# Kernel optimization log

Hardware: AMD Instinct MI355X
Metric: run time of the kernel (lower is better)

The kernel has to match this reference:

```python
import jax, jax.numpy as jnp
import numpy as np

N = 100000  # nodes
E = 1600000  # edges (without self-loops)


def _gcn_norm(edge_index, n):
    # add self loops, compute symmetric normalization D^-1/2 (A+I) D^-1/2
    loops = jnp.arange(n, dtype=edge_index.dtype)
    src = jnp.concatenate([edge_index[0], loops])
    dst = jnp.concatenate([edge_index[1], loops])
    deg = jax.ops.segment_sum(jnp.ones_like(dst, dtype=jnp.float32), dst, num_segments=n)
    dinv = jax.lax.rsqrt(jnp.maximum(deg, 1.0))  # deg >= 1 due to self loops
    norm = dinv[src] * dinv[dst]  # [E+N]
    return src, dst, norm


def _gcn_layer(x, W, b, src, dst, norm, n):
    h = x @ W  # [N, out]
    msg = h[src] * norm[:, None]  # [E+N, out]
    agg = jax.ops.segment_sum(msg, dst, num_segments=n)
    return agg + b


def setup_inputs() -> dict:
    key = jax.random.key(0)
    ks = jax.random.split(key, 8)
    x = jax.random.normal(ks[0], (N, 256), dtype=jnp.float32)
    edge_index = jax.random.randint(ks[1], (2, E), 0, N, dtype=jnp.int32)
    W1 = jax.random.normal(ks[2], (256, 128), dtype=jnp.float32) / np.sqrt(256.0)
    b1 = jnp.zeros((128,), dtype=jnp.float32)
    W2 = jax.random.normal(ks[3], (128, 128), dtype=jnp.float32) / np.sqrt(128.0)
    b2 = jnp.zeros((128,), dtype=jnp.float32)
    W3 = jax.random.normal(ks[4], (128, 16), dtype=jnp.float32) / np.sqrt(128.0)
    b3 = jnp.zeros((16,), dtype=jnp.float32)
    return {"x": x, "edge_index": edge_index, "W1": W1, "b1": b1,
            "W2": W2, "b2": b2, "W3": W3, "b3": b3}


def reference(x, edge_index, W1, b1, W2, b2, W3, b3):
    n = x.shape[0]
    src, dst, norm = _gcn_norm(edge_index, n)
    h = jax.nn.relu(_gcn_layer(x, W1, b1, src, dst, norm, n))
    # dropout layers are identity in eval mode
    h = jax.nn.relu(_gcn_layer(h, W2, b2, src, dst, norm, n))
    out = _gcn_layer(h, W3, b3, src, dst, norm, n)
    return out
```

## Files before the change

### kernel.cpp

```cpp
#include <hip/hip_runtime.h>
#include <hip/hip_bf16.h>
#include <cstdint>
#include <cstddef>

typedef __hip_bfloat16 bf16;

typedef __attribute__((ext_vector_type(8))) short s16x8;
typedef __attribute__((ext_vector_type(4))) float f32x4;
typedef __attribute__((ext_vector_type(8))) unsigned short u16x8;

__device__ __forceinline__ float bflo(unsigned u) { return __uint_as_float(u << 16); }
__device__ __forceinline__ float bfhi(unsigned u) { return __uint_as_float(u & 0xffff0000u); }
__device__ __forceinline__ unsigned packbf2(float a, float b) {
  unsigned lo = (unsigned)__bfloat16_as_ushort(__float2bfloat16(a));
  unsigned hi = (unsigned)__bfloat16_as_ushort(__float2bfloat16(b));
  return lo | (hi << 16);
}
__device__ __forceinline__ float to_f(float v) { return v; }
__device__ __forceinline__ float to_f(bf16 v) { return __bfloat162float(v); }

__device__ __forceinline__ void gload_lds16(const void* g, void* l) {
  __builtin_amdgcn_global_load_lds((const __attribute__((address_space(1))) unsigned int*)g,
                                   (__attribute__((address_space(3))) unsigned int*)l, 16, 0, 0);
}

__global__ __launch_bounds__(256) void k_detect(const unsigned* __restrict__ x, int* __restrict__ flag,
                                                int forced) {
  __shared__ int sm[256];
  int t = threadIdx.x;
  if (forced >= 0) { if (t == 0) *flag = forced; return; }
  int cnt = 0;
  for (int i = t; i < 4096; i += 256) {
    unsigned u = x[i];
    unsigned lo_exp = (u >> 7) & 0xFF;
    cnt += (lo_exp >= 97 && lo_exp <= 130) ? 1 : 0;
  }
  sm[t] = cnt;
  __syncthreads();
  for (int off = 128; off > 0; off >>= 1) {
    if (t < off) sm[t] += sm[t + off];
    __syncthreads();
  }
  if (t == 0) *flag = (sm[0] > 2048) ? 1 : 0;
}


__global__ __launch_bounds__(256) void k_init(int* fil, int* rcur, int n) {
  int i = blockIdx.x * 256 + threadIdx.x;
  if (i < n) fil[i] = 0;
  if (blockIdx.x == 0 && threadIdx.x < 8) rcur[threadIdx.x] = 0;
}

template <int P>
__global__ __launch_bounds__(256) void k_bin(const int* __restrict__ src, const int* __restrict__ dst,
                                             uint2* __restrict__ stage, int* __restrict__ rcur,
                                             int* __restrict__ fil, int* __restrict__ csr,
                                             int E, int N, int rsz, int capR, int cap) {
  __shared__ int hcnt[P], hbase[P], hcur[P];
  const int t = threadIdx.x;
  const int base = blockIdx.x * 2048;
  if (t < P) hcnt[t] = 0;
  __syncthreads();
  int dloc[8], sloc[8], rloc[8];
#pragma unroll
  for (int j = 0; j < 8; ++j) {
    int e = base + j * 256 + t;
    bool valid = (e < E);
    int d = valid ? dst[e] : 0;
    int s = valid ? src[e] : 0;
    if ((unsigned)d >= (unsigned)N) valid = false;
    if ((unsigned)s >= (unsigned)N) s = 0;
    int r = valid ? (d / rsz) : -1;
    dloc[j] = d; sloc[j] = s; rloc[j] = r;
    if (valid) atomicAdd(&hcnt[r], 1);
  }
  __syncthreads();
  if (t < P) {
    hbase[t] = atomicAdd(&rcur[t], hcnt[t]);
    hcur[t] = 0;
  }
  __syncthreads();
#pragma unroll
  for (int j = 0; j < 8; ++j) {
    int r = rloc[j];
    if (r >= 0) {
      int pos = hbase[r] + atomicAdd(&hcur[r], 1);
      if (pos < capR) {
        stage[(size_t)r * capR + pos] = make_uint2((unsigned)dloc[j], (unsigned)sloc[j]);
      } else {
        int pp = atomicAdd(&fil[dloc[j]], 1);
        if (pp < cap) csr[(size_t)dloc[j] * cap + pp] = sloc[j];
      }
    }
  }
}

template <int P>
__global__ __launch_bounds__(256) void k_fillb(const uint2* __restrict__ stage, const int* __restrict__ rcur,
                                               int* __restrict__ fil, int* __restrict__ csr,
                                               int capR, int cap) {
  const int r = blockIdx.x & (P - 1);
  const int nb = gridDim.x / P;
  const int chunk = blockIdx.x / P;
  int cnt = rcur[r];
  if (cnt > capR) cnt = capR;
  const uint2* sg = stage + (size_t)r * capR;
  for (int i = chunk * 256 + threadIdx.x; i < cnt; i += nb * 256) {
    uint2 e = sg[i];
    int p = atomicAdd(&fil[e.x], 1);
    if (p < cap) csr[(size_t)e.x * cap + p] = (int)e.y;
  }
}

__global__ __launch_bounds__(256) void k_dinv(const int* __restrict__ fil, float* __restrict__ dinv, int n) {
  int i = blockIdx.x * 256 + threadIdx.x;
  if (i < n) dinv[i] = rsqrtf((float)fil[i] + 1.0f);
}

template <typename TB, int WANT, int SPLIT>
__global__ __launch_bounds__(256) void k_packB(const int* __restrict__ flag,
                                               const TB* __restrict__ B,
                                               unsigned short* __restrict__ Bp, int K) {
  if (*flag != WANT) return;
  const int nf = (K >> 5) * 512;
  int t = blockIdx.x * 256 + threadIdx.x;
  if (t >= nf) return;
  int s = t >> 9, rem = t & 511, c = rem >> 6, l = rem & 63;
  int kb = (s << 5) + ((l >> 4) << 3);
  int col = (c << 4) + (l & 15);
  u16x8 vh, vl;
#pragma unroll
  for (int i = 0; i < 8; ++i) {
    float f = to_f(B[(size_t)(kb + i) * 128 + col]);
    bf16 h = __float2bfloat16(f);
    vh[i] = __bfloat16_as_ushort(h);
    if (SPLIT) {
      float r = f - __bfloat162float(h);
      vl[i] = __bfloat16_as_ushort(__float2bfloat16(r));
    }
  }
  *(u16x8*)(Bp + (size_t)t * 8) = vh;
  if (SPLIT) *(u16x8*)(Bp + ((size_t)nf + t) * 8) = vl;
}

template <typename TA, int WANT, int MODE, int KT>
__global__ __launch_bounds__(256) void k_gemm_mfma(const int* __restrict__ flag,
                                                   const TA* __restrict__ A,
                                                   const unsigned short* __restrict__ Bp,
                                                   const float* __restrict__ dinv,
                                                   bf16* __restrict__ C, int M) {
  if (*flag != WANT) return;
  constexpr int steps = KT >> 5;
  constexpr int NFRAG = (MODE >= 1) ? 16 : 8;
  constexpr int FPW = NFRAG / 4;
  constexpr size_t nfbytes = (size_t)steps * 8192;
  __shared__ s16x8 lds[2][NFRAG * 64];
  const int tid = threadIdx.x;
  const int l = tid & 63;
  const int w = tid >> 6;
  const int row0 = blockIdx.x * 128 + w * 32;
  int arow0 = row0 + (l & 15);
  int arow1 = row0 + 16 + (l & 15);
  if (arow0 >= M) arow0 = M - 1;
  if (arow1 >= M) arow1 = M - 1;
  const TA* Ap0 = A + (size_t)arow0 * KT + ((l >> 4) << 3);
  const TA* Ap1 = A + (size_t)arow1 * KT + ((l >> 4) << 3);
  const char* Bb = (const char*)Bp;

  auto stage = [&](int b, int s) {
#pragma unroll
    for (int j = 0; j < FPW; ++j) {
      int q = w * FPW + j;
      size_t off = (q < 8) ? ((size_t)(s * 8 + q)) * 1024
                           : nfbytes + ((size_t)(s * 8 + q - 8)) * 1024;
      gload_lds16(Bb + off + (size_t)l * 16, (void*)&lds[b][q * 64]);
    }
  };

  f32x4 acc[2][8];
#pragma unroll
  for (int rs = 0; rs < 2; ++rs)
#pragma unroll
    for (int c = 0; c < 8; ++c) acc[rs][c] = (f32x4){0.f, 0.f, 0.f, 0.f};

  float4 f0[3], f1[3], f2[3], f3[3];
  s16x8 ra0[3], ra1[3];
  auto loadA = [&](int s, int slot) {
    if constexpr (MODE == 2) {
      const float* p0 = (const float*)(Ap0 + (s << 5));
      const float* p1 = (const float*)(Ap1 + (s << 5));
      f0[slot] = *(const float4*)p0; f1[slot] = *(const float4*)(p0 + 4);
      f2[slot] = *(const float4*)p1; f3[slot] = *(const float4*)(p1 + 4);
    } else {
      ra0[slot] = *(const s16x8*)(Ap0 + (s << 5));
      ra1[slot] = *(const s16x8*)(Ap1 + (s << 5));
    }
  };

  auto mkfrag = [&](const float4& lo4, const float4& hi4, s16x8& a, s16x8& alo) {
    float f[8] = {lo4.x, lo4.y, lo4.z, lo4.w, hi4.x, hi4.y, hi4.z, hi4.w};
#pragma unroll
    for (int i = 0; i < 8; ++i) {
      bf16 h = __float2bfloat16(f[i]);
      a[i] = (short)__bfloat16_as_ushort(h);
      float r = f[i] - __bfloat162float(h);
      alo[i] = (short)__bfloat16_as_ushort(__float2bfloat16(r));
    }
  };

  stage(0, 0);
  __builtin_amdgcn_sched_barrier(0);
  loadA(0, 0);
  if constexpr (steps > 1) loadA(1, 1);
  if constexpr (MODE == 2) asm volatile("s_waitcnt vmcnt(8)" ::: "memory");
  else                     asm volatile("s_waitcnt vmcnt(4)" ::: "memory");
  __builtin_amdgcn_s_barrier();
  __builtin_amdgcn_sched_barrier(0);

#pragma unroll
  for (int s = 0; s < steps; ++s) {
    const int b = s & 1;
    if (s + 1 < steps) stage(b ^ 1, s + 1);
    __builtin_amdgcn_sched_barrier(0);
    if (s + 2 < steps) loadA(s + 2, (s + 2) % 3);
    s16x8 a0, alo0, a1, alo1;
    if constexpr (MODE == 2) {
      const int sl = s % 3;
      mkfrag(f0[sl], f1[sl], a0, alo0);
      mkfrag(f2[sl], f3[sl], a1, alo1);
    } else {
      a0 = ra0[s % 3];
      a1 = ra1[s % 3];
    }
#pragma unroll
    for (int c = 0; c < 8; ++c) {
      s16x8 bh = lds[b][c * 64 + l];
      acc[0][c] = __builtin_amdgcn_mfma_f32_16x16x32_bf16(a0, bh, acc[0][c], 0, 0, 0);
      acc[1][c] = __builtin_amdgcn_mfma_f32_16x16x32_bf16(a1, bh, acc[1][c], 0, 0, 0);
      if constexpr (MODE >= 1) {
        s16x8 bl = lds[b][(8 + c) * 64 + l];
        acc[0][c] = __builtin_amdgcn_mfma_f32_16x16x32_bf16(a0, bl, acc[0][c], 0, 0, 0);
        acc[1][c] = __builtin_amdgcn_mfma_f32_16x16x32_bf16(a1, bl, acc[1][c], 0, 0, 0);
      }
      if constexpr (MODE == 2) {
        acc[0][c] = __builtin_amdgcn_mfma_f32_16x16x32_bf16(alo0, bh, acc[0][c], 0, 0, 0);
        acc[1][c] = __builtin_amdgcn_mfma_f32_16x16x32_bf16(alo1, bh, acc[1][c], 0, 0, 0);
      }
    }
    if (s + 1 < steps) {
      if (s + 2 < steps) {
        if constexpr (MODE == 2) asm volatile("s_waitcnt vmcnt(4)" ::: "memory");
        else                     asm volatile("s_waitcnt vmcnt(2)" ::: "memory");
      } else {
        asm volatile("s_waitcnt vmcnt(0)" ::: "memory");
      }
      __builtin_amdgcn_s_barrier();
      __builtin_amdgcn_sched_barrier(0);
    }
  }

  const int lb = l & 15;
#pragma unroll
  for (int rs = 0; rs < 2; ++rs) {
    const int rbase = row0 + rs * 16 + ((l >> 4) << 2);
#pragma unroll
    for (int r = 0; r < 4; ++r) {
      int row = rbase + r;
      if (row < M) {
        float sc = dinv[row];
        bf16* Cr = C + (size_t)row * 128 + lb;
#pragma unroll
        for (int c = 0; c < 8; ++c) Cr[c << 4] = __float2bfloat16(acc[rs][c][r] * sc);
      }
    }
  }
}

template <typename TB, int WANT>
__global__ __launch_bounds__(256) void k_gemm16(const int* __restrict__ flag,
                                                const bf16* __restrict__ A, const TB* __restrict__ B,
                                                const float* __restrict__ dinv, float* __restrict__ C, int M) {
  if (*flag != WANT) return;
  __shared__ float Bs[128][16];
  const int tid = threadIdx.x;
  for (int l = tid; l < 128 * 16; l += 256) Bs[l >> 4][l & 15] = to_f(B[l]);
  __syncthreads();
  const int r = blockIdx.x * 64 + (tid >> 2);
  const int c0 = (tid & 3) * 4;
  if (r >= M) return;
  const bf16* Ar = A + (size_t)r * 128;
  float a0 = 0.f, a1 = 0.f, a2 = 0.f, a3 = 0.f;
#pragma unroll
  for (int k = 0; k < 128; k += 8) {
    uint4 u = *(const uint4*)&Ar[k];
    float f[8] = {bflo(u.x), bfhi(u.x), bflo(u.y), bfhi(u.y),
                  bflo(u.z), bfhi(u.z), bflo(u.w), bfhi(u.w)};
#pragma unroll
    for (int j = 0; j < 8; ++j) {
      float4 b = *(const float4*)&Bs[k + j][c0];
      a0 = fmaf(f[j], b.x, a0); a1 = fmaf(f[j], b.y, a1);
      a2 = fmaf(f[j], b.z, a2); a3 = fmaf(f[j], b.w, a3);
    }
  }
  float s = dinv[r];
  *(float4*)&C[(size_t)r * 16 + c0] = make_float4(a0 * s, a1 * s, a2 * s, a3 * s);
}


template <typename TB, int WANT>
__global__ __launch_bounds__(256) void k_agg128(const int* __restrict__ flag,
                                                const bf16* __restrict__ Hs, const int* __restrict__ deg,
                                                const int* __restrict__ csr, const float* __restrict__ dinv,
                                                const TB* __restrict__ bias, bf16* __restrict__ out,
                                                int M, int cap) {
  if (*flag != WANT) return;
  const int wid = threadIdx.x >> 6, lane = threadIdx.x & 63;
  const int node = blockIdx.x * 4 + wid;
  if (node >= M) return;
  const int g = lane >> 4, li = lane & 15;
  int dg = deg[node];
  if (dg > cap) dg = cap;
  const int* ce = csr + (size_t)node * cap;
  const int total = dg + 1;
  float acc[8];
#pragma unroll
  for (int i = 0; i < 8; ++i) acc[i] = 0.f;

  auto rowsrc = [&](int k) -> int {
    return (k == 0) ? node : ce[k - 1];
  };
  auto addu4 = [&](uint4 u) {
    acc[0] += bflo(u.x); acc[1] += bfhi(u.x);
    acc[2] += bflo(u.y); acc[3] += bfhi(u.y);
    acc[4] += bflo(u.z); acc[5] += bfhi(u.z);
    acc[6] += bflo(u.w); acc[7] += bfhi(u.w);
  };

  int base = 0;
  for (; base + 8 <= total; base += 8) {
    int s0 = rowsrc(base + g);
    int s1 = rowsrc(base + 4 + g);
    uint4 u0 = *(const uint4*)(Hs + (size_t)s0 * 128 + li * 8);
    uint4 u1 = *(const uint4*)(Hs + (size_t)s1 * 128 + li * 8);
    addu4(u0); addu4(u1);
  }
  for (; base < total; base += 4) {
    int k = base + g;
    bool v = (k < total);
    int s = v ? rowsrc(k) : node;
    uint4 u = *(const uint4*)(Hs + (size_t)s * 128 + li * 8);
    if (v) addu4(u);
  }

#pragma unroll
  for (int i = 0; i < 8; ++i) {
    acc[i] += __shfl_xor(acc[i], 16);
    acc[i] += __shfl_xor(acc[i], 32);
  }

  if (lane < 16) {
    float di = dinv[node];
    const int c0 = li * 8;
    float o[8];
#pragma unroll
    for (int i = 0; i < 8; ++i) o[i] = fmaxf(acc[i] * di + to_f(bias[c0 + i]), 0.f);
    uint4 ov;
    ov.x = packbf2(o[0], o[1]);
    ov.y = packbf2(o[2], o[3]);
    ov.z = packbf2(o[4], o[5]);
    ov.w = packbf2(o[6], o[7]);
    *(uint4*)(out + (size_t)node * 128 + c0) = ov;
  }
}

template <typename TB, typename TO, int WANT>
__global__ __launch_bounds__(256) void k_agg16(const int* __restrict__ flag,
                                               const float* __restrict__ Hs, const int* __restrict__ deg,
                                               const int* __restrict__ csr, const float* __restrict__ dinv,
                                               const TB* __restrict__ bias, TO* __restrict__ out,
                                               int M, int cap) {
  if (*flag != WANT) return;
  int sub = threadIdx.x >> 4, lane = threadIdx.x & 15;
  int node = blockIdx.x * 16 + sub;
  if (node >= M) return;
  float acc = Hs[(size_t)node * 16 + lane];
  int dg = deg[node];
  if (dg > cap) dg = cap;
  const int* ce = csr + (size_t)node * cap;
  int e = 0;
  for (; e + 8 <= dg; e += 8) {
    int s0 = ce[e],     s1 = ce[e + 1], s2 = ce[e + 2], s3 = ce[e + 3];
    int s4 = ce[e + 4], s5 = ce[e + 5], s6 = ce[e + 6], s7 = ce[e + 7];
    acc += (Hs[(size_t)s0 * 16 + lane] + Hs[(size_t)s1 * 16 + lane]) +
           (Hs[(size_t)s2 * 16 + lane] + Hs[(size_t)s3 * 16 + lane]) +
           (Hs[(size_t)s4 * 16 + lane] + Hs[(size_t)s5 * 16 + lane]) +
           (Hs[(size_t)s6 * 16 + lane] + Hs[(size_t)s7 * 16 + lane]);
  }
  for (; e + 4 <= dg; e += 4) {
    int s0 = ce[e], s1 = ce[e + 1], s2 = ce[e + 2], s3 = ce[e + 3];
    acc += Hs[(size_t)s0 * 16 + lane] + Hs[(size_t)s1 * 16 + lane] +
           Hs[(size_t)s2 * 16 + lane] + Hs[(size_t)s3 * 16 + lane];
  }
  for (; e < dg; ++e) acc += Hs[(size_t)ce[e] * 16 + lane];
  float o = acc * dinv[node] + to_f(bias[lane]);
  out[(size_t)node * 16 + lane] = (TO)o;
}


extern "C" void kernel_launch(void* const* d_in, const int* in_sizes, int n_in,
                              void* d_out, int out_size, void* d_ws, size_t ws_size,
                              hipStream_t stream) {
  const int* ei = (const int*)d_in[1];

  const long long w1sz = in_sizes[2];
  const int kmode = (int)(w1sz / 32768);
  const int N = (int)((long long)in_sizes[0] * 128 / w1sz);
  const int E = (kmode == 1) ? in_sizes[1] / 2 : in_sizes[1] / 8;
  const int forced = (kmode == 2) ? 1 : (kmode == 4) ? 0 : -1;
  const int* srcv = ei;
  const int* dstv = ei + E;

  long long meandeg = (N > 0) ? (long long)E / N : 0;
  int cap = (int)((4 * meandeg + 15) & ~15LL);
  if (cap < 64) cap = 64;

  char* p = (char*)d_ws;
  auto alloc = [&](size_t b) { char* r = p; p += (b + 255) & ~(size_t)255; return r; };
  int*   flag   = (int*)alloc(256);
  int*   rcur   = (int*)alloc(256);
  int*   fil    = (int*)alloc((size_t)N * 4);
  float* dinv   = (float*)alloc((size_t)N * 4);
  int*   csr    = (int*)alloc((size_t)N * cap * 4);
  bf16*  HsB    = (bf16*)alloc((size_t)N * 128 * 2);
  bf16*  hB     = (bf16*)alloc((size_t)N * 128 * 2);
  unsigned short* Bp1 = (unsigned short*)alloc(131072);
  unsigned short* Bp2 = (unsigned short*)alloc(65536);
  float* Hs16   = (float*)HsB;
  uint2* stg    = (uint2*)HsB;
  const int capR = N * 4;

  const int gN = (N + 255) / 256;
  k_detect<<<1, 256, 0, stream>>>((const unsigned*)d_in[0], flag, forced);
  k_init <<<gN, 256, 0, stream>>>(fil, rcur, N);
  {
    constexpr int P = 8;
    const int rsz = (N + P - 1) / P;
    const int nch = (E + 2047) / 2048;
    k_bin<P>  <<<nch, 256, 0, stream>>>(srcv, dstv, stg, rcur, fil, csr, E, N, rsz, capR, cap);
    k_fillb<P><<<1024, 256, 0, stream>>>(stg, rcur, fil, csr, capR, cap);
  }
  k_dinv <<<gN, 256, 0, stream>>>(fil, dinv, N);

  const int gM128 = (N + 127) / 128;
  const int gM64  = (N + 63) / 64;
  const int gAgg  = (N + 3) / 4;
  const bool doB16 = (forced != 0);
  const bool doF32 = (forced != 1);

  if (doB16) {
    const bf16* x  = (const bf16*)d_in[0];
    const bf16* b1 = (const bf16*)d_in[3];
    const bf16* b2 = (const bf16*)d_in[5];
    const bf16* W3 = (const bf16*)d_in[6]; const bf16* b3 = (const bf16*)d_in[7];
    k_packB<bf16, 1, 0><<<16, 256, 0, stream>>>(flag, (const bf16*)d_in[2], Bp1, 256);
    k_packB<bf16, 1, 0><<<8,  256, 0, stream>>>(flag, (const bf16*)d_in[4], Bp2, 128);
    k_gemm_mfma<bf16, 1, 0, 256><<<gM128, 256, 0, stream>>>(flag, x, Bp1, dinv, HsB, N);
    k_agg128<bf16, 1><<<gAgg, 256, 0, stream>>>(flag, HsB, fil, csr, dinv, b1, hB, N, cap);
    k_gemm_mfma<bf16, 1, 0, 128><<<gM128, 256, 0, stream>>>(flag, hB, Bp2, dinv, HsB, N);
    k_agg128<bf16, 1><<<gAgg, 256, 0, stream>>>(flag, HsB, fil, csr, dinv, b2, hB, N, cap);
    k_gemm16<bf16, 1><<<gM64, 256, 0, stream>>>(flag, hB, W3, dinv, Hs16, N);
    k_agg16<bf16, bf16, 1><<<(N + 15) / 16, 256, 0, stream>>>(flag, Hs16, fil, csr, dinv, b3,
                                                              (bf16*)d_out, N, cap);
  }
  if (doF32) {
    const float* x  = (const float*)d_in[0];
    const float* b1 = (const float*)d_in[3];
    const float* b2 = (const float*)d_in[5];
    const float* W3 = (const float*)d_in[6]; const float* b3 = (const float*)d_in[7];
    k_packB<float, 0, 1><<<16, 256, 0, stream>>>(flag, (const float*)d_in[2], Bp1, 256);
    k_packB<float, 0, 1><<<8,  256, 0, stream>>>(flag, (const float*)d_in[4], Bp2, 128);
    k_gemm_mfma<float, 0, 2, 256><<<gM128, 256, 0, stream>>>(flag, x, Bp1, dinv, HsB, N);
    k_agg128<float, 0><<<gAgg, 256, 0, stream>>>(flag, HsB, fil, csr, dinv, b1, hB, N, cap);
    k_gemm_mfma<bf16, 0, 1, 128><<<gM128, 256, 0, stream>>>(flag, hB, Bp2, dinv, HsB, N);
    k_agg128<float, 0><<<gAgg, 256, 0, stream>>>(flag, HsB, fil, csr, dinv, b2, hB, N, cap);
    k_gemm16<float, 0><<<gM64, 256, 0, stream>>>(flag, hB, W3, dinv, Hs16, N);
    k_agg16<float, float, 0><<<(N + 15) / 16, 256, 0, stream>>>(flag, Hs16, fil, csr, dinv, b3,
                                                                (float*)d_out, N, cap);
  }
}
```

Baseline: 493.3 us.

## Fuse layer-1 GEMM with edge binning and move dinv scaling into aggregation

Layer 1's GEMM no longer depends on dinv: the per-row source scaling moves from the GEMM epilogue into the aggregation kernels, which now multiply each gathered row by dinv[src]. That lets the first GEMM run in the same grid as the edge-binning kernel, so compute-bound and atomic-bound work overlap. The duplicated bf16 and f32 launch sequences become a single sequence that branches on the device flag inside each kernel, and the two weight-packing kernels are merged into one, cutting the launch count roughly in half. In exchange, aggregation does an extra dinv gather per edge, and the binning stage buffer moves to hB so the GEMM output can live in HsB.

```diff
diff --git a/kernel.cpp b/kernel.cpp
--- a/kernel.cpp
+++ b/kernel.cpp
@@ -44,21 +44,176 @@
   if (t == 0) *flag = (sm[0] > 2048) ? 1 : 0;
 }
 
-
 __global__ __launch_bounds__(256) void k_init(int* fil, int* rcur, int n) {
   int i = blockIdx.x * 256 + threadIdx.x;
   if (i < n) fil[i] = 0;
   if (blockIdx.x == 0 && threadIdx.x < 8) rcur[threadIdx.x] = 0;
 }
 
+__device__ __forceinline__ void pack_body(const void* Bsrc, unsigned short* Bp, int K,
+                                          int isb, int t) {
+  const int nf = (K >> 5) * 512;
+  if (t >= nf) return;
+  int s = t >> 9, rem = t & 511, c = rem >> 6, l = rem & 63;
+  int kb = (s << 5) + ((l >> 4) << 3);
+  int col = (c << 4) + (l & 15);
+  u16x8 vh, vl;
+#pragma unroll
+  for (int i = 0; i < 8; ++i) {
+    float f = isb ? to_f(((const bf16*)Bsrc)[(size_t)(kb + i) * 128 + col])
+                  : ((const float*)Bsrc)[(size_t)(kb + i) * 128 + col];
+    bf16 h = __float2bfloat16(f);
+    vh[i] = __bfloat16_as_ushort(h);
+    float r = f - __bfloat162float(h);
+    vl[i] = __bfloat16_as_ushort(__float2bfloat16(r));
+  }
+  *(u16x8*)(Bp + (size_t)t * 8) = vh;
+  if (!isb) *(u16x8*)(Bp + ((size_t)nf + t) * 8) = vl;
+}
+
+__global__ __launch_bounds__(256) void k_pack(const int* __restrict__ flag,
+                                              const void* __restrict__ B1, const void* __restrict__ B2,
+                                              unsigned short* __restrict__ Bp1,
+                                              unsigned short* __restrict__ Bp2) {
+  const int isb = (*flag == 1);
+  if (blockIdx.x < 16) pack_body(B1, Bp1, 256, isb, blockIdx.x * 256 + threadIdx.x);
+  else                 pack_body(B2, Bp2, 128, isb, (blockIdx.x - 16) * 256 + threadIdx.x);
+}
+
+template <typename TA, int MODE, int KT>
+__device__ void gemm_body(const TA* __restrict__ A, const unsigned short* __restrict__ Bp,
+                          bf16* __restrict__ C, int M, int blk, s16x8* ldsbuf) {
+  constexpr int steps = KT >> 5;
+  constexpr int NFRAG = (MODE >= 1) ? 16 : 8;
+  constexpr int FPW = NFRAG / 4;
+  constexpr size_t nfbytes = (size_t)steps * 8192;
+  const int tid = threadIdx.x;
+  const int l = tid & 63;
+  const int w = tid >> 6;
+  const int row0 = blk * 128 + w * 32;
+  int arow0 = row0 + (l & 15);
+  int arow1 = row0 + 16 + (l & 15);
+  if (arow0 >= M) arow0 = M - 1;
+  if (arow1 >= M) arow1 = M - 1;
+  const TA* Ap0 = A + (size_t)arow0 * KT + ((l >> 4) << 3);
+  const TA* Ap1 = A + (size_t)arow1 * KT + ((l >> 4) << 3);
+  const char* Bb = (const char*)Bp;
+
+  auto stage = [&](int b, int s) {
+#pragma unroll
+    for (int j = 0; j < FPW; ++j) {
+      int q = w * FPW + j;
+      size_t off = (q < 8) ? ((size_t)(s * 8 + q)) * 1024
+                           : nfbytes + ((size_t)(s * 8 + q - 8)) * 1024;
+      gload_lds16(Bb + off + (size_t)l * 16, (void*)&ldsbuf[b * (NFRAG * 64) + q * 64]);
+    }
+  };
+
+  f32x4 acc[2][8];
+#pragma unroll
+  for (int rs = 0; rs < 2; ++rs)
+#pragma unroll
+    for (int c = 0; c < 8; ++c) acc[rs][c] = (f32x4){0.f, 0.f, 0.f, 0.f};
+
+  float4 f0[3], f1[3], f2[3], f3[3];
+  s16x8 ra0[3], ra1[3];
+  auto loadA = [&](int s, int slot) {
+    if constexpr (MODE == 2) {
+      const float* p0 = (const float*)(Ap0 + (s << 5));
+      const float* p1 = (const float*)(Ap1 + (s << 5));
+      f0[slot] = *(const float4*)p0; f1[slot] = *(const float4*)(p0 + 4);
+      f2[slot] = *(const float4*)p1; f3[slot] = *(const float4*)(p1 + 4);
+    } else {
+      ra0[slot] = *(const s16x8*)(Ap0 + (s << 5));
+      ra1[slot] = *(const s16x8*)(Ap1 + (s << 5));
+    }
+  };
+  auto mkfrag = [&](const float4& lo4, const float4& hi4, s16x8& a, s16x8& alo) {
+    float f[8] = {lo4.x, lo4.y, lo4.z, lo4.w, hi4.x, hi4.y, hi4.z, hi4.w};
+#pragma unroll
+    for (int i = 0; i < 8; ++i) {
+      bf16 h = __float2bfloat16(f[i]);
+      a[i] = (short)__bfloat16_as_ushort(h);
+      float r = f[i] - __bfloat162float(h);
+      alo[i] = (short)__bfloat16_as_ushort(__float2bfloat16(r));
+    }
+  };
+
+  stage(0, 0);
+  __builtin_amdgcn_sched_barrier(0);
+  loadA(0, 0);
+  if constexpr (steps > 1) loadA(1, 1);
+  if constexpr (MODE == 2) asm volatile("s_waitcnt vmcnt(8)" ::: "memory");
+  else                     asm volatile("s_waitcnt vmcnt(4)" ::: "memory");
+  __builtin_amdgcn_s_barrier();
+  __builtin_amdgcn_sched_barrier(0);
+
+#pragma unroll
+  for (int s = 0; s < steps; ++s) {
+    const int b = s & 1;
+    if (s + 1 < steps) stage(b ^ 1, s + 1);
+    __builtin_amdgcn_sched_barrier(0);
+    if (s + 2 < steps) loadA(s + 2, (s + 2) % 3);
+    s16x8 a0, alo0, a1, alo1;
+    if constexpr (MODE == 2) {
+      const int sl = s % 3;
+      mkfrag(f0[sl], f1[sl], a0, alo0);
+      mkfrag(f2[sl], f3[sl], a1, alo1);
+    } else {
+      a0 = ra0[s % 3];
+      a1 = ra1[s % 3];
+    }
+#pragma unroll
+    for (int c = 0; c < 8; ++c) {
+      s16x8 bh = ldsbuf[b * (NFRAG * 64) + c * 64 + l];
+      acc[0][c] = __builtin_amdgcn_mfma_f32_16x16x32_bf16(a0, bh, acc[0][c], 0, 0, 0);
+      acc[1][c] = __builtin_amdgcn_mfma_f32_16x16x32_bf16(a1, bh, acc[1][c], 0, 0, 0);
+      if constexpr (MODE >= 1) {
+        s16x8 bl = ldsbuf[b * (NFRAG * 64) + (8 + c) * 64 + l];
+        acc[0][c] = __builtin_amdgcn_mfma_f32_16x16x32_bf16(a0, bl, acc[0][c], 0, 0, 0);
+        acc[1][c] = __builtin_amdgcn_mfma_f32_16x16x32_bf16(a1, bl, acc[1][c], 0, 0, 0);
+      }
+      if constexpr (MODE == 2) {
+        acc[0][c] = __builtin_amdgcn_mfma_f32_16x16x32_bf16(alo0, bh, acc[0][c], 0, 0, 0);
+        acc[1][c] = __builtin_amdgcn_mfma_f32_16x16x32_bf16(alo1, bh, acc[1][c], 0, 0, 0);
+      }
+    }
+    if (s + 1 < steps) {
+      if (s + 2 < steps) {
+        if constexpr (MODE == 2) asm volatile("s_waitcnt vmcnt(4)" ::: "memory");
+        else                     asm volatile("s_waitcnt vmcnt(2)" ::: "memory");
+      } else {
+        asm volatile("s_waitcnt vmcnt(0)" ::: "memory");
+      }
+      __builtin_amdgcn_s_barrier();
+      __builtin_amdgcn_sched_barrier(0);
+    }
+  }
+
+  const int lb = l & 15;
+#pragma unroll
+  for (int rs = 0; rs < 2; ++rs) {
+    const int rbase = row0 + rs * 16 + ((l >> 4) << 2);
+#pragma unroll
+    for (int r = 0; r < 4; ++r) {
+      int row = rbase + r;
+      if (row < M) {
+        bf16* Cr = C + (size_t)row * 128 + lb;
+#pragma unroll
+        for (int c = 0; c < 8; ++c) Cr[c << 4] = __float2bfloat16(acc[rs][c][r]);
+      }
+    }
+  }
+}
+
 template <int P>
-__global__ __launch_bounds__(256) void k_bin(const int* __restrict__ src, const int* __restrict__ dst,
-                                             uint2* __restrict__ stage, int* __restrict__ rcur,
-                                             int* __restrict__ fil, int* __restrict__ csr,
-                                             int E, int N, int rsz, int capR, int cap) {
-  __shared__ int hcnt[P], hbase[P], hcur[P];
+__device__ void bin_body(const int* __restrict__ src, const int* __restrict__ dst,
+                         uint2* __restrict__ stage, int* __restrict__ rcur,
+                         int* __restrict__ fil, int* __restrict__ csr,
+                         int E, int N, int rsz, int capR, int cap, int bid,
+                         int* hcnt, int* hbase, int* hcur) {
   const int t = threadIdx.x;
-  const int base = blockIdx.x * 2048;
+  const int base = bid * 2048;
   if (t < P) hcnt[t] = 0;
   __syncthreads();
   int dloc[8], sloc[8], rloc[8];
@@ -93,6 +248,36 @@
       }
     }
   }
+}
+
+template <int P>
+__global__ __launch_bounds__(256) void k_g1bin(const int* __restrict__ flag,
+                                               const void* __restrict__ A,
+                                               const unsigned short* __restrict__ Bp1,
+                                               bf16* __restrict__ C, int M,
+                                               const int* __restrict__ src, const int* __restrict__ dst,
+                                               uint2* __restrict__ stage, int* __restrict__ rcur,
+                                               int* __restrict__ fil, int* __restrict__ csr,
+                                               int E, int N, int rsz, int capR, int cap,
+                                               int gemmBlocks) {
+  __shared__ s16x8 lds[2 * 16 * 64];
+  __shared__ int hcnt[P], hbase[P], hcur[P];
+  if ((int)blockIdx.x < gemmBlocks) {
+    if (*flag == 1) gemm_body<bf16, 0, 256>((const bf16*)A, Bp1, C, M, blockIdx.x, lds);
+    else            gemm_body<float, 2, 256>((const float*)A, Bp1, C, M, blockIdx.x, lds);
+  } else {
+    bin_body<P>(src, dst, stage, rcur, fil, csr, E, N, rsz, capR, cap,
+                blockIdx.x - gemmBlocks, hcnt, hbase, hcur);
+  }
+}
+
+__global__ __launch_bounds__(256) void k_gemm2(const int* __restrict__ flag,
+                                               const bf16* __restrict__ A,
+                                               const unsigned short* __restrict__ Bp2,
+                                               bf16* __restrict__ C, int M) {
+  __shared__ s16x8 lds[2 * 16 * 64];
+  if (*flag == 1) gemm_body<bf16, 0, 128>(A, Bp2, C, M, blockIdx.x, lds);
+  else            gemm_body<bf16, 1, 128>(A, Bp2, C, M, blockIdx.x, lds);
 }
 
 template <int P>
@@ -117,203 +302,12 @@
   if (i < n) dinv[i] = rsqrtf((float)fil[i] + 1.0f);
 }
 
-template <typename TB, int WANT, int SPLIT>
-__global__ __launch_bounds__(256) void k_packB(const int* __restrict__ flag,
-                                               const TB* __restrict__ B,
-                                               unsigned short* __restrict__ Bp, int K) {
-  if (*flag != WANT) return;
-  const int nf = (K >> 5) * 512;
-  int t = blockIdx.x * 256 + threadIdx.x;
-  if (t >= nf) return;
-  int s = t >> 9, rem = t & 511, c = rem >> 6, l = rem & 63;
-  int kb = (s << 5) + ((l >> 4) << 3);
-  int col = (c << 4) + (l & 15);
-  u16x8 vh, vl;
-#pragma unroll
-  for (int i = 0; i < 8; ++i) {
-    float f = to_f(B[(size_t)(kb + i) * 128 + col]);
-    bf16 h = __float2bfloat16(f);
-    vh[i] = __bfloat16_as_ushort(h);
-    if (SPLIT) {
-      float r = f - __bfloat162float(h);
-      vl[i] = __bfloat16_as_ushort(__float2bfloat16(r));
-    }
-  }
-  *(u16x8*)(Bp + (size_t)t * 8) = vh;
-  if (SPLIT) *(u16x8*)(Bp + ((size_t)nf + t) * 8) = vl;
-}
-
-template <typename TA, int WANT, int MODE, int KT>
-__global__ __launch_bounds__(256) void k_gemm_mfma(const int* __restrict__ flag,
-                                                   const TA* __restrict__ A,
-                                                   const unsigned short* __restrict__ Bp,
-                                                   const float* __restrict__ dinv,
-                                                   bf16* __restrict__ C, int M) {
-  if (*flag != WANT) return;
-  constexpr int steps = KT >> 5;
-  constexpr int NFRAG = (MODE >= 1) ? 16 : 8;
-  constexpr int FPW = NFRAG / 4;
-  constexpr size_t nfbytes = (size_t)steps * 8192;
-  __shared__ s16x8 lds[2][NFRAG * 64];
-  const int tid = threadIdx.x;
-  const int l = tid & 63;
-  const int w = tid >> 6;
-  const int row0 = blockIdx.x * 128 + w * 32;
-  int arow0 = row0 + (l & 15);
-  int arow1 = row0 + 16 + (l & 15);
-  if (arow0 >= M) arow0 = M - 1;
-  if (arow1 >= M) arow1 = M - 1;
-  const TA* Ap0 = A + (size_t)arow0 * KT + ((l >> 4) << 3);
-  const TA* Ap1 = A + (size_t)arow1 * KT + ((l >> 4) << 3);
-  const char* Bb = (const char*)Bp;
-
-  auto stage = [&](int b, int s) {
-#pragma unroll
-    for (int j = 0; j < FPW; ++j) {
-      int q = w * FPW + j;
-      size_t off = (q < 8) ? ((size_t)(s * 8 + q)) * 1024
-                           : nfbytes + ((size_t)(s * 8 + q - 8)) * 1024;
-      gload_lds16(Bb + off + (size_t)l * 16, (void*)&lds[b][q * 64]);
-    }
-  };
-
-  f32x4 acc[2][8];
-#pragma unroll
-  for (int rs = 0; rs < 2; ++rs)
-#pragma unroll
-    for (int c = 0; c < 8; ++c) acc[rs][c] = (f32x4){0.f, 0.f, 0.f, 0.f};
-
-  float4 f0[3], f1[3], f2[3], f3[3];
-  s16x8 ra0[3], ra1[3];
-  auto loadA = [&](int s, int slot) {
-    if constexpr (MODE == 2) {
-      const float* p0 = (const float*)(Ap0 + (s << 5));
-      const float* p1 = (const float*)(Ap1 + (s << 5));
-      f0[slot] = *(const float4*)p0; f1[slot] = *(const float4*)(p0 + 4);
-      f2[slot] = *(const float4*)p1; f3[slot] = *(const float4*)(p1 + 4);
-    } else {
-      ra0[slot] = *(const s16x8*)(Ap0 + (s << 5));
-      ra1[slot] = *(const s16x8*)(Ap1 + (s << 5));
-    }
-  };
-
-  auto mkfrag = [&](const float4& lo4, const float4& hi4, s16x8& a, s16x8& alo) {
-    float f[8] = {lo4.x, lo4.y, lo4.z, lo4.w, hi4.x, hi4.y, hi4.z, hi4.w};
-#pragma unroll
-    for (int i = 0; i < 8; ++i) {
-      bf16 h = __float2bfloat16(f[i]);
-      a[i] = (short)__bfloat16_as_ushort(h);
-      float r = f[i] - __bfloat162float(h);
-      alo[i] = (short)__bfloat16_as_ushort(__float2bfloat16(r));
-    }
-  };
-
-  stage(0, 0);
-  __builtin_amdgcn_sched_barrier(0);
-  loadA(0, 0);
-  if constexpr (steps > 1) loadA(1, 1);
-  if constexpr (MODE == 2) asm volatile("s_waitcnt vmcnt(8)" ::: "memory");
-  else                     asm volatile("s_waitcnt vmcnt(4)" ::: "memory");
-  __builtin_amdgcn_s_barrier();
-  __builtin_amdgcn_sched_barrier(0);
-
-#pragma unroll
-  for (int s = 0; s < steps; ++s) {
-    const int b = s & 1;
-    if (s + 1 < steps) stage(b ^ 1, s + 1);
-    __builtin_amdgcn_sched_barrier(0);
-    if (s + 2 < steps) loadA(s + 2, (s + 2) % 3);
-    s16x8 a0, alo0, a1, alo1;
-    if constexpr (MODE == 2) {
-      const int sl = s % 3;
-      mkfrag(f0[sl], f1[sl], a0, alo0);
-      mkfrag(f2[sl], f3[sl], a1, alo1);
-    } else {
-      a0 = ra0[s % 3];
-      a1 = ra1[s % 3];
-    }
-#pragma unroll
-    for (int c = 0; c < 8; ++c) {
-      s16x8 bh = lds[b][c * 64 + l];
-      acc[0][c] = __builtin_amdgcn_mfma_f32_16x16x32_bf16(a0, bh, acc[0][c], 0, 0, 0);
-      acc[1][c] = __builtin_amdgcn_mfma_f32_16x16x32_bf16(a1, bh, acc[1][c], 0, 0, 0);
-      if constexpr (MODE >= 1) {
-        s16x8 bl = lds[b][(8 + c) * 64 + l];
-        acc[0][c] = __builtin_amdgcn_mfma_f32_16x16x32_bf16(a0, bl, acc[0][c], 0, 0, 0);
-        acc[1][c] = __builtin_amdgcn_mfma_f32_16x16x32_bf16(a1, bl, acc[1][c], 0, 0, 0);
-      }
-      if constexpr (MODE == 2) {
-        acc[0][c] = __builtin_amdgcn_mfma_f32_16x16x32_bf16(alo0, bh, acc[0][c], 0, 0, 0);
-        acc[1][c] = __builtin_amdgcn_mfma_f32_16x16x32_bf16(alo1, bh, acc[1][c], 0, 0, 0);
-      }
-    }
-    if (s + 1 < steps) {
-      if (s + 2 < steps) {
-        if constexpr (MODE == 2) asm volatile("s_waitcnt vmcnt(4)" ::: "memory");
-        else                     asm volatile("s_waitcnt vmcnt(2)" ::: "memory");
-      } else {
-        asm volatile("s_waitcnt vmcnt(0)" ::: "memory");
-      }
-      __builtin_amdgcn_s_barrier();
-      __builtin_amdgcn_sched_barrier(0);
-    }
-  }
-
-  const int lb = l & 15;
-#pragma unroll
-  for (int rs = 0; rs < 2; ++rs) {
-    const int rbase = row0 + rs * 16 + ((l >> 4) << 2);
-#pragma unroll
-    for (int r = 0; r < 4; ++r) {
-      int row = rbase + r;
-      if (row < M) {
-        float sc = dinv[row];
-        bf16* Cr = C + (size_t)row * 128 + lb;
-#pragma unroll
-        for (int c = 0; c < 8; ++c) Cr[c << 4] = __float2bfloat16(acc[rs][c][r] * sc);
-      }
-    }
-  }
-}
-
-template <typename TB, int WANT>
-__global__ __launch_bounds__(256) void k_gemm16(const int* __restrict__ flag,
-                                                const bf16* __restrict__ A, const TB* __restrict__ B,
-                                                const float* __restrict__ dinv, float* __restrict__ C, int M) {
-  if (*flag != WANT) return;
-  __shared__ float Bs[128][16];
-  const int tid = threadIdx.x;
-  for (int l = tid; l < 128 * 16; l += 256) Bs[l >> 4][l & 15] = to_f(B[l]);
-  __syncthreads();
-  const int r = blockIdx.x * 64 + (tid >> 2);
-  const int c0 = (tid & 3) * 4;
-  if (r >= M) return;
-  const bf16* Ar = A + (size_t)r * 128;
-  float a0 = 0.f, a1 = 0.f, a2 = 0.f, a3 = 0.f;
-#pragma unroll
-  for (int k = 0; k < 128; k += 8) {
-    uint4 u = *(const uint4*)&Ar[k];
-    float f[8] = {bflo(u.x), bfhi(u.x), bflo(u.y), bfhi(u.y),
-                  bflo(u.z), bfhi(u.z), bflo(u.w), bfhi(u.w)};
-#pragma unroll
-    for (int j = 0; j < 8; ++j) {
-      float4 b = *(const float4*)&Bs[k + j][c0];
-      a0 = fmaf(f[j], b.x, a0); a1 = fmaf(f[j], b.y, a1);
-      a2 = fmaf(f[j], b.z, a2); a3 = fmaf(f[j], b.w, a3);
-    }
-  }
-  float s = dinv[r];
-  *(float4*)&C[(size_t)r * 16 + c0] = make_float4(a0 * s, a1 * s, a2 * s, a3 * s);
-}
-
-
-template <typename TB, int WANT>
 __global__ __launch_bounds__(256) void k_agg128(const int* __restrict__ flag,
                                                 const bf16* __restrict__ Hs, const int* __restrict__ deg,
                                                 const int* __restrict__ csr, const float* __restrict__ dinv,
-                                                const TB* __restrict__ bias, bf16* __restrict__ out,
+                                                const void* __restrict__ bias, bf16* __restrict__ out,
                                                 int M, int cap) {
-  if (*flag != WANT) return;
+  const int isb = (*flag == 1);
   const int wid = threadIdx.x >> 6, lane = threadIdx.x & 63;
   const int node = blockIdx.x * 4 + wid;
   if (node >= M) return;
@@ -326,14 +320,12 @@
 #pragma unroll
   for (int i = 0; i < 8; ++i) acc[i] = 0.f;
 
-  auto rowsrc = [&](int k) -> int {
-    return (k == 0) ? node : ce[k - 1];
-  };
-  auto addu4 = [&](uint4 u) {
-    acc[0] += bflo(u.x); acc[1] += bfhi(u.x);
-    acc[2] += bflo(u.y); acc[3] += bfhi(u.y);
-    acc[4] += bflo(u.z); acc[5] += bfhi(u.z);
-    acc[6] += bflo(u.w); acc[7] += bfhi(u.w);
+  auto rowsrc = [&](int k) -> int { return (k == 0) ? node : ce[k - 1]; };
+  auto addu4 = [&](uint4 u, float ds) {
+    acc[0] = fmaf(bflo(u.x), ds, acc[0]); acc[1] = fmaf(bfhi(u.x), ds, acc[1]);
+    acc[2] = fmaf(bflo(u.y), ds, acc[2]); acc[3] = fmaf(bfhi(u.y), ds, acc[3]);
+    acc[4] = fmaf(bflo(u.z), ds, acc[4]); acc[5] = fmaf(bfhi(u.z), ds, acc[5]);
+    acc[6] = fmaf(bflo(u.w), ds, acc[6]); acc[7] = fmaf(bfhi(u.w), ds, acc[7]);
   };
 
   int base = 0;
@@ -342,14 +334,16 @@
     int s1 = rowsrc(base + 4 + g);
     uint4 u0 = *(const uint4*)(Hs + (size_t)s0 * 128 + li * 8);
     uint4 u1 = *(const uint4*)(Hs + (size_t)s1 * 128 + li * 8);
-    addu4(u0); addu4(u1);
+    float d0 = dinv[s0], d1 = dinv[s1];
+    addu4(u0, d0); addu4(u1, d1);
   }
   for (; base < total; base += 4) {
     int k = base + g;
     bool v = (k < total);
     int s = v ? rowsrc(k) : node;
     uint4 u = *(const uint4*)(Hs + (size_t)s * 128 + li * 8);
-    if (v) addu4(u);
+    float ds = dinv[s];
+    if (v) addu4(u, ds);
   }
 
 #pragma unroll
@@ -363,7 +357,10 @@
     const int c0 = li * 8;
     float o[8];
 #pragma unroll
-    for (int i = 0; i < 8; ++i) o[i] = fmaxf(acc[i] * di + to_f(bias[c0 + i]), 0.f);
+    for (int i = 0; i < 8; ++i) {
+      float bv = isb ? to_f(((const bf16*)bias)[c0 + i]) : ((const float*)bias)[c0 + i];
+      o[i] = fmaxf(acc[i] * di + bv, 0.f);
+    }
     uint4 ov;
     ov.x = packbf2(o[0], o[1]);
     ov.y = packbf2(o[2], o[3]);
@@ -373,37 +370,64 @@
   }
 }
 
-template <typename TB, typename TO, int WANT>
+__global__ __launch_bounds__(256) void k_gemm16(const int* __restrict__ flag,
+                                                const bf16* __restrict__ A, const void* __restrict__ B,
+                                                float* __restrict__ C, int M) {
+  const int isb = (*flag == 1);
+  __shared__ float Bs[128][16];
+  const int tid = threadIdx.x;
+  for (int l = tid; l < 128 * 16; l += 256)
+    Bs[l >> 4][l & 15] = isb ? to_f(((const bf16*)B)[l]) : ((const float*)B)[l];
+  __syncthreads();
+  const int r = blockIdx.x * 64 + (tid >> 2);
+  const int c0 = (tid & 3) * 4;
+  if (r >= M) return;
+  const bf16* Ar = A + (size_t)r * 128;
+  float a0 = 0.f, a1 = 0.f, a2 = 0.f, a3 = 0.f;
+#pragma unroll
+  for (int k = 0; k < 128; k += 8) {
+    uint4 u = *(const uint4*)&Ar[k];
+    float f[8] = {bflo(u.x), bfhi(u.x), bflo(u.y), bfhi(u.y),
+                  bflo(u.z), bfhi(u.z), bflo(u.w), bfhi(u.w)};
+#pragma unroll
+    for (int j = 0; j < 8; ++j) {
+      float4 b = *(const float4*)&Bs[k + j][c0];
+      a0 = fmaf(f[j], b.x, a0); a1 = fmaf(f[j], b.y, a1);
+      a2 = fmaf(f[j], b.z, a2); a3 = fmaf(f[j], b.w, a3);
+    }
+  }
+  *(float4*)&C[(size_t)r * 16 + c0] = make_float4(a0, a1, a2, a3);
+}
+
 __global__ __launch_bounds__(256) void k_agg16(const int* __restrict__ flag,
                                                const float* __restrict__ Hs, const int* __restrict__ deg,
                                                const int* __restrict__ csr, const float* __restrict__ dinv,
-                                               const TB* __restrict__ bias, TO* __restrict__ out,
+                                               const void* __restrict__ bias, void* __restrict__ out,
                                                int M, int cap) {
-  if (*flag != WANT) return;
+  const int isb = (*flag == 1);
   int sub = threadIdx.x >> 4, lane = threadIdx.x & 15;
   int node = blockIdx.x * 16 + sub;
   if (node >= M) return;
-  float acc = Hs[(size_t)node * 16 + lane];
+  float acc = Hs[(size_t)node * 16 + lane] * dinv[node];
   int dg = deg[node];
   if (dg > cap) dg = cap;
   const int* ce = csr + (size_t)node * cap;
   int e = 0;
-  for (; e + 8 <= dg; e += 8) {
-    int s0 = ce[e],     s1 = ce[e + 1], s2 = ce[e + 2], s3 = ce[e + 3];
-    int s4 = ce[e + 4], s5 = ce[e + 5], s6 = ce[e + 6], s7 = ce[e + 7];
-    acc += (Hs[(size_t)s0 * 16 + lane] + Hs[(size_t)s1 * 16 + lane]) +
-           (Hs[(size_t)s2 * 16 + lane] + Hs[(size_t)s3 * 16 + lane]) +
-           (Hs[(size_t)s4 * 16 + lane] + Hs[(size_t)s5 * 16 + lane]) +
-           (Hs[(size_t)s6 * 16 + lane] + Hs[(size_t)s7 * 16 + lane]);
-  }
   for (; e + 4 <= dg; e += 4) {
     int s0 = ce[e], s1 = ce[e + 1], s2 = ce[e + 2], s3 = ce[e + 3];
-    acc += Hs[(size_t)s0 * 16 + lane] + Hs[(size_t)s1 * 16 + lane] +
-           Hs[(size_t)s2 * 16 + lane] + Hs[(size_t)s3 * 16 + lane];
-  }
-  for (; e < dg; ++e) acc += Hs[(size_t)ce[e] * 16 + lane];
-  float o = acc * dinv[node] + to_f(bias[lane]);
-  out[(size_t)node * 16 + lane] = (TO)o;
+    acc = fmaf(Hs[(size_t)s0 * 16 + lane], dinv[s0], acc);
+    acc = fmaf(Hs[(size_t)s1 * 16 + lane], dinv[s1], acc);
+    acc = fmaf(Hs[(size_t)s2 * 16 + lane], dinv[s2], acc);
+    acc = fmaf(Hs[(size_t)s3 * 16 + lane], dinv[s3], acc);
+  }
+  for (; e < dg; ++e) {
+    int s = ce[e];
+    acc = fmaf(Hs[(size_t)s * 16 + lane], dinv[s], acc);
+  }
+  float bv = isb ? to_f(((const bf16*)bias)[lane]) : ((const float*)bias)[lane];
+  float o = acc * dinv[node] + bv;
+  if (isb) ((bf16*)out)[(size_t)node * 16 + lane] = (bf16)o;
+  else     ((float*)out)[(size_t)node * 16 + lane] = o;
 }
 
 
@@ -436,55 +460,28 @@
   unsigned short* Bp1 = (unsigned short*)alloc(131072);
   unsigned short* Bp2 = (unsigned short*)alloc(65536);
   float* Hs16   = (float*)HsB;
-  uint2* stg    = (uint2*)HsB;
+  uint2* stg    = (uint2*)hB;
   const int capR = N * 4;
 
   const int gN = (N + 255) / 256;
-  k_detect<<<1, 256, 0, stream>>>((const unsigned*)d_in[0], flag, forced);
-  k_init <<<gN, 256, 0, stream>>>(fil, rcur, N);
-  {
-    constexpr int P = 8;
-    const int rsz = (N + P - 1) / P;
-    const int nch = (E + 2047) / 2048;
-    k_bin<P>  <<<nch, 256, 0, stream>>>(srcv, dstv, stg, rcur, fil, csr, E, N, rsz, capR, cap);
-    k_fillb<P><<<1024, 256, 0, stream>>>(stg, rcur, fil, csr, capR, cap);
-  }
-  k_dinv <<<gN, 256, 0, stream>>>(fil, dinv, N);
-
   const int gM128 = (N + 127) / 128;
   const int gM64  = (N + 63) / 64;
   const int gAgg  = (N + 3) / 4;
-  const bool doB16 = (forced != 0);
-  const bool doF32 = (forced != 1);
-
-  if (doB16) {
-    const bf16* x  = (const bf16*)d_in[0];
-    const bf16* b1 = (const bf16*)d_in[3];
-    const bf16* b2 = (const bf16*)d_in[5];
-    const bf16* W3 = (const bf16*)d_in[6]; const bf16* b3 = (const bf16*)d_in[7];
-    k_packB<bf16, 1, 0><<<16, 256, 0, stream>>>(flag, (const bf16*)d_in[2], Bp1, 256);
-    k_packB<bf16, 1, 0><<<8,  256, 0, stream>>>(flag, (const bf16*)d_in[4], Bp2, 128);
-    k_gemm_mfma<bf16, 1, 0, 256><<<gM128, 256, 0, stream>>>(flag, x, Bp1, dinv, HsB, N);
-    k_agg128<bf16, 1><<<gAgg, 256, 0, stream>>>(flag, HsB, fil, csr, dinv, b1, hB, N, cap);
-    k_gemm_mfma<bf16, 1, 0, 128><<<gM128, 256, 0, stream>>>(flag, hB, Bp2, dinv, HsB, N);
-    k_agg128<bf16, 1><<<gAgg, 256, 0, stream>>>(flag, HsB, fil, csr, dinv, b2, hB, N, cap);
-    k_gemm16<bf16, 1><<<gM64, 256, 0, stream>>>(flag, hB, W3, dinv, Hs16, N);
-    k_agg16<bf16, bf16, 1><<<(N + 15) / 16, 256, 0, stream>>>(flag, Hs16, fil, csr, dinv, b3,
-                                                              (bf16*)d_out, N, cap);
-  }
-  if (doF32) {
-    const float* x  = (const float*)d_in[0];
-    const float* b1 = (const float*)d_in[3];
-    const float* b2 = (const float*)d_in[5];
-    const float* W3 = (const float*)d_in[6]; const float* b3 = (const float*)d_in[7];
-    k_packB<float, 0, 1><<<16, 256, 0, stream>>>(flag, (const float*)d_in[2], Bp1, 256);
-    k_packB<float, 0, 1><<<8,  256, 0, stream>>>(flag, (const float*)d_in[4], Bp2, 128);
-    k_gemm_mfma<float, 0, 2, 256><<<gM128, 256, 0, stream>>>(flag, x, Bp1, dinv, HsB, N);
-    k_agg128<float, 0><<<gAgg, 256, 0, stream>>>(flag, HsB, fil, csr, dinv, b1, hB, N, cap);
-    k_gemm_mfma<bf16, 0, 1, 128><<<gM128, 256, 0, stream>>>(flag, hB, Bp2, dinv, HsB, N);
-    k_agg128<float, 0><<<gAgg, 256, 0, stream>>>(flag, HsB, fil, csr, dinv, b2, hB, N, cap);
-    k_gemm16<float, 0><<<gM64, 256, 0, stream>>>(flag, hB, W3, dinv, Hs16, N);
-    k_agg16<float, float, 0><<<(N + 15) / 16, 256, 0, stream>>>(flag, Hs16, fil, csr, dinv, b3,
-                                                                (float*)d_out, N, cap);
-  }
-}
+  constexpr int P = 8;
+  const int rsz = (N + P - 1) / P;
+  const int nch = (E + 2047) / 2048;
+
+  k_detect<<<1, 256, 0, stream>>>((const unsigned*)d_in[0], flag, forced);
+  k_init  <<<gN, 256, 0, stream>>>(fil, rcur, N);
+  k_pack  <<<24, 256, 0, stream>>>(flag, d_in[2], d_in[4], Bp1, Bp2);
+  k_g1bin<P><<<gM128 + nch, 256, 0, stream>>>(flag, d_in[0], Bp1, HsB, N,
+                                              srcv, dstv, stg, rcur, fil, csr,
+                                              E, N, rsz, capR, cap, gM128);
+  k_fillb<P><<<1024, 256, 0, stream>>>(stg, rcur, fil, csr, capR, cap);
+  k_dinv  <<<gN, 256, 0, stream>>>(fil, dinv, N);
+  k_agg128<<<gAgg, 256, 0, stream>>>(flag, HsB, fil, csr, dinv, d_in[3], hB, N, cap);
+  k_gemm2 <<<gM128, 256, 0, stream>>>(flag, hB, Bp2, HsB, N);
+  k_agg128<<<gAgg, 256, 0, stream>>>(flag, HsB, fil, csr, dinv, d_in[5], hB, N, cap);
+  k_gemm16<<<gM64, 256, 0, stream>>>(flag, hB, d_in[6], Hs16, N);
+  k_agg16 <<<(N + 15) / 16, 256, 0, stream>>>(flag, Hs16, fil, csr, dinv, d_in[7], d_out, N, cap);
+}
```

Result: faster. 474.6 us (-3.8%).
